# Kernel optimization log

Hardware: AMD Instinct MI355X
Metric: run time of the kernel (lower is better)

Reference implementation:

```python
import jax, jax.numpy as jnp
import numpy as np
import math

N, E, H, NB, NL, NG, NELEM = 50000, 800000, 64, 8, 2, 64, 100
CUTOFF = 5.0


def _lin(k, fin, fout):
    kw, kb = jax.random.split(k)
    bound = 1.0 / math.sqrt(fin)
    w = jax.random.uniform(kw, (fin, fout), jnp.float32, -bound, bound)
    b = jax.random.uniform(kb, (fout,), jnp.float32, -bound, bound)
    return w, b


def setup_inputs() -> dict:
    key = jax.random.key(0)
    ks = jax.random.split(key, 12)
    z = jax.random.randint(ks[0], (N,), 0, NELEM)
    pos = jax.random.normal(ks[1], (N, 3), jnp.float32)
    edge_index = jax.random.randint(ks[2], (2, E), 0, N)
    batch = jnp.sort(jax.random.randint(ks[3], (N,), 0, NG))
    embed = jax.random.normal(ks[4], (NELEM, H), jnp.float32)
    # stacked per-interaction MLP params, leading dim = NL
    msg_w1, msg_b1, msg_w2, msg_b2 = [], [], [], []
    upd_w1, upd_b1, upd_w2, upd_b2 = [], [], [], []
    for l in range(NL):
        kl = jax.random.fold_in(ks[5], l)
        k1, k2, k3, k4 = jax.random.split(kl, 4)
        w, b = _lin(k1, 2 * H + NB, H); msg_w1.append(w); msg_b1.append(b)
        w, b = _lin(k2, H, H); msg_w2.append(w); msg_b2.append(b)
        w, b = _lin(k3, 2 * H, H); upd_w1.append(w); upd_b1.append(b)
        w, b = _lin(k4, H, H); upd_w2.append(w); upd_b2.append(b)
    eh_w1, eh_b1 = _lin(ks[6], H, H)
    eh_w2, eh_b2 = _lin(ks[7], H, 1)
    return {
        "z": z, "pos": pos, "edge_index": edge_index, "batch": batch,
        "embed": embed,
        "msg_w1": jnp.stack(msg_w1), "msg_b1": jnp.stack(msg_b1),
        "msg_w2": jnp.stack(msg_w2), "msg_b2": jnp.stack(msg_b2),
        "upd_w1": jnp.stack(upd_w1), "upd_b1": jnp.stack(upd_b1),
        "upd_w2": jnp.stack(upd_w2), "upd_b2": jnp.stack(upd_b2),
        "eh_w1": eh_w1, "eh_b1": eh_b1, "eh_w2": eh_w2, "eh_b2": eh_b2,
    }


def _mace_energy(pos, embed, msg_w1, msg_b1, msg_w2, msg_b2,
                 upd_w1, upd_b1, upd_w2, upd_b2,
                 eh_w1, eh_b1, eh_w2, eh_b2,
                 z, edge_index, batch):
    row, col = edge_index[0], edge_index[1]
    edge_vec = pos[row] - pos[col]                      # (E,3)
    d = jnp.linalg.norm(edge_vec, axis=-1)              # (E,)
    env = jnp.where(d < CUTOFF,
                    jnp.cos(d * (math.pi / (2 * CUTOFF))) ** 2,
                    0.0)
    freqs = jnp.arange(1, NB + 1, dtype=pos.dtype) * (math.pi / CUTOFF)
    d_safe = jnp.where(d > 0, d, 1.0)[:, None]
    edge_attr = jnp.sin(freqs * d[:, None]) / d_safe * env[:, None]  # (E,NB)

    x = embed[z]                                        # (N,H)
    for l in range(NL):
        # PyG source_to_target: x_j = x[row], x_i = x[col], aggregate at col
        msg_in = jnp.concatenate([x[col], x[row], edge_attr], axis=-1)  # (E,2H+NB)
        m = jax.nn.silu(msg_in @ msg_w1[l] + msg_b1[l]) @ msg_w2[l] + msg_b2[l]
        agg = jax.ops.segment_sum(m, col, num_segments=N)               # (N,H)
        u_in = jnp.concatenate([x, agg], axis=-1)
        upd = jax.nn.silu(u_in @ upd_w1[l] + upd_b1[l]) @ upd_w2[l] + upd_b2[l]
        x = x + upd

    atomic_e = jax.nn.silu(x @ eh_w1 + eh_b1) @ eh_w2 + eh_b2           # (N,1)
    energy = jax.ops.segment_sum(atomic_e, batch, num_segments=NG)      # (NG,1)
    return energy.squeeze(-1)


def reference(z, pos, edge_index, batch, embed,
              msg_w1, msg_b1, msg_w2, msg_b2,
              upd_w1, upd_b1, upd_w2, upd_b2,
              eh_w1, eh_b1, eh_w2, eh_b2):
    return _mace_energy(pos, embed, msg_w1, msg_b1, msg_w2, msg_b2,
                        upd_w1, upd_b1, upd_w2, upd_b2,
                        eh_w1, eh_b1, eh_w2, eh_b2,
                        z, edge_index, batch)
```

## Files before the change

kernel.cpp:

```cpp
#include <hip/hip_runtime.h>
#include <math.h>

#define NN 50000
#define EE 800000
#define HH 64
#define NBASIS 8
#define NLAYER 2
#define NGRAPH 64
#define NBLK1 49

using half2_t = decltype(__builtin_amdgcn_cvt_pkrtz(0.0f, 0.0f));
typedef _Float16 f16x8 __attribute__((ext_vector_type(8)));
typedef float f32x4 __attribute__((ext_vector_type(4)));

union U4H8 { uint4 u; f16x8 h; };

__device__ __forceinline__ float silu_f(float v) {
    return v * (1.0f / (1.0f + __expf(-v)));
}

__device__ __forceinline__ unsigned pk2(float a, float b) {
    union { half2_t h; unsigned u; } x;
    x.h = __builtin_amdgcn_cvt_pkrtz(a, b);
    return x.u;
}

__global__ __launch_bounds__(256) void prep_k(
    const int* __restrict__ z, const float* __restrict__ embed,
    float* __restrict__ x, unsigned* __restrict__ xh,
    const float* __restrict__ msg_w1, const float* __restrict__ msg_w2,
    const float* __restrict__ upd_w1, const float* __restrict__ upd_w2,
    const float* __restrict__ eh_w1,
    unsigned* __restrict__ w1t, unsigned* __restrict__ w2t,
    unsigned* __restrict__ w1tu, unsigned* __restrict__ w2tu,
    unsigned* __restrict__ ehw1t,
    const int* __restrict__ ecol, int* __restrict__ deg)
{
    int b = blockIdx.x;
    if (b < 6250) {
        int idx = b * 256 + threadIdx.x;
        int n = idx >> 5;
        int p = idx & 31;
        const float2* er = (const float2*)(embed + ((size_t)z[n] << 6));
        float2 v = er[p];
        ((float2*)x)[idx] = v;
        xh[idx] = pk2(v.x, v.y);
    } else if (b < 6362) {
        int idx = (b - 6250) * 256 + threadIdx.x;
        if (idx < 10240) {
            int l = idx / 5120, rem = idx % 5120;
            int f = rem / 80, kp = rem % 80;
            const float* w = msg_w1 + (size_t)l * 136 * 64;
            unsigned v = 0;
            if (kp < 68) v = pk2(w[(2*kp)*64 + f], w[(2*kp+1)*64 + f]);
            w1t[idx] = v;
        } else if (idx < 14336) {
            int j = idx - 10240;
            int l = j / 2048, rem = j % 2048;
            int n = rem / 32, kp = rem % 32;
            const float* w = msg_w2 + (size_t)l * 64 * 64;
            w2t[j] = pk2(w[(2*kp)*64 + n], w[(2*kp+1)*64 + n]);
        } else if (idx < 22528) {
            int j = idx - 14336;
            int l = j / 4096, rem = j % 4096;
            int f = rem >> 6, kp = rem & 63;
            const float* w = upd_w1 + (size_t)l * 128 * 64;
            w1tu[j] = pk2(w[(2*kp)*64 + f], w[(2*kp+1)*64 + f]);
        } else if (idx < 26624) {
            int j = idx - 22528;
            int l = j / 2048, rem = j % 2048;
            int n = rem / 32, kp = rem % 32;
            const float* w = upd_w2 + (size_t)l * 64 * 64;
            w2tu[j] = pk2(w[(2*kp)*64 + n], w[(2*kp+1)*64 + n]);
        } else if (idx < 28672) {
            int j = idx - 26624;
            int f = j / 32, kp = j % 32;
            ehw1t[j] = pk2(eh_w1[(2*kp)*64 + f], eh_w1[(2*kp+1)*64 + f]);
        }
    } else {
        int e = (b - 6362) * 256 + threadIdx.x;
        if (e < EE) atomicAdd(&deg[ecol[e]], 1);
    }
}

__global__ __launch_bounds__(1024) void scan1_k(
    const int* __restrict__ deg, int* __restrict__ cursor,
    int* __restrict__ bsum)
{
    __shared__ int wsum[16];
    int t = threadIdx.x, lane = t & 63, wave = t >> 6;
    int i = blockIdx.x * 1024 + t;
    int v = (i < NN) ? deg[i] : 0;
    int s = v;
#pragma unroll
    for (int off = 1; off < 64; off <<= 1) {
        int tv = __shfl_up(s, off, 64);
        if (lane >= off) s += tv;
    }
    if (lane == 63) wsum[wave] = s;
    __syncthreads();
    if (wave == 0) {
        int ws = (lane < 16) ? wsum[lane] : 0;
        int ss = ws;
#pragma unroll
        for (int off = 1; off < 16; off <<= 1) {
            int tv = __shfl_up(ss, off, 64);
            if (lane >= off) ss += tv;
        }
        if (lane < 16) wsum[lane] = ss - ws;
    }
    __syncthreads();
    int excl = wsum[wave] + s - v;
    if (i < NN) cursor[i] = excl;
    if (t == 1023) bsum[blockIdx.x] = excl + v;
}

__global__ __launch_bounds__(64) void scan2_k(int* __restrict__ bsum)
{
    int lane = threadIdx.x;
    int v = (lane < NBLK1) ? bsum[lane] : 0;
    int s = v;
#pragma unroll
    for (int off = 1; off < 64; off <<= 1) {
        int tv = __shfl_up(s, off, 64);
        if (lane >= off) s += tv;
    }
    if (lane < NBLK1) bsum[lane] = s - v;
}

__global__ __launch_bounds__(256) void scatter_k(
    const int* __restrict__ erow, const int* __restrict__ ecol,
    const float* __restrict__ pos,
    int* __restrict__ cursor, const int* __restrict__ bsum,
    uint4* __restrict__ edgeS)
{
    int e = blockIdx.x * 256 + threadIdx.x;
    if (e >= EE) return;
    int c = ecol[e], r = erow[e];
    int slot = atomicAdd(&cursor[c], 1) + bsum[c >> 10];
    float dx = pos[3*r]   - pos[3*c];
    float dy = pos[3*r+1] - pos[3*c+1];
    float dz = pos[3*r+2] - pos[3*c+2];
    float d = sqrtf(dx*dx + dy*dy + dz*dz);
    uint4 v;
    v.x = (unsigned)r; v.y = (unsigned)c;
    v.z = __float_as_uint(d); v.w = 0;
    edgeS[slot] = v;
}

__global__ __launch_bounds__(256, 4) void msg_k(
    const uint4* __restrict__ edgeS,
    const unsigned* __restrict__ xh,
    const unsigned* __restrict__ w1t, const float* __restrict__ b1,
    const unsigned* __restrict__ w2t, const float* __restrict__ b2,
    float* __restrict__ agg)
{
    __shared__ __align__(16) unsigned earr[4][64 * 4];
    __shared__ int ckey_s[4][64];
    __shared__ int rkey_s[4][64];
    __shared__ float Mbuf[4][64 * 33];

    const int wid  = threadIdx.x >> 6;
    const int lane = threadIdx.x & 63;
    const int q = lane >> 4, n15 = lane & 15;
    const size_t base = (size_t)blockIdx.x * 256 + wid * 64;

    {
        uint4 ev = edgeS[base + lane];
        rkey_s[wid][lane] = (int)ev.x;
        ckey_s[wid][lane] = (int)ev.y;
        float d = __uint_as_float(ev.z);
        float env = 0.0f;
        if (d < 5.0f) {
            float cv = __cosf(d * 0.31415926535897932f);
            env = cv * cv;
        }
        float scale = (d > 0.0f) ? (env / d) : env;
        float ea[NBASIS];
#pragma unroll
        for (int k = 0; k < NBASIS; ++k)
            ea[k] = __sinf((float)(k + 1) * 0.62831853071795865f * d) * scale;
#pragma unroll
        for (int p = 0; p < 4; ++p)
            earr[wid][lane * 4 + p] = pk2(ea[2*p], ea[2*p+1]);
    }
    __syncthreads();

    int cn[4], rn[4];
#pragma unroll
    for (int nt = 0; nt < 4; ++nt) {
        int eB = nt * 16 + n15;
        cn[nt] = ckey_s[wid][eB];
        rn[nt] = rkey_s[wid][eB];
    }

    f32x4 acc1[4][4];
#pragma unroll
    for (int mt = 0; mt < 4; ++mt) {
        f32x4 binit = *(const f32x4*)(b1 + mt * 16 + q * 4);
#pragma unroll
        for (int nt = 0; nt < 4; ++nt) acc1[mt][nt] = binit;
    }
#pragma unroll
    for (int ks = 0; ks < 5; ++ks) {
        U4H8 bfk[4];
#pragma unroll
        for (int nt = 0; nt < 4; ++nt) {
            if (ks == 4) {
                uint4 zz; zz.x = zz.y = zz.z = zz.w = 0;
                bfk[nt].u = (q == 0) ? *(const uint4*)(earr[wid] + (nt * 16 + n15) * 4) : zz;
            } else if (ks < 2) {
                bfk[nt].u = ((const uint4*)(xh + ((size_t)cn[nt] << 5)))[ks * 4 + q];
            } else {
                bfk[nt].u = ((const uint4*)(xh + ((size_t)rn[nt] << 5)))[(ks - 2) * 4 + q];
            }
        }
#pragma unroll
        for (int mt = 0; mt < 4; ++mt) {
            U4H8 af;
            af.u = *(const uint4*)(w1t + (size_t)(mt * 16 + n15) * 80 + ks * 16 + q * 4);
#pragma unroll
            for (int nt = 0; nt < 4; ++nt)
                acc1[mt][nt] = __builtin_amdgcn_mfma_f32_16x16x32_f16(
                    af.h, bfk[nt].h, acc1[mt][nt], 0, 0, 0);
        }
    }

    unsigned psrc[4][4][2];
#pragma unroll
    for (int mt = 0; mt < 4; ++mt)
#pragma unroll
        for (int nt = 0; nt < 4; ++nt) {
            psrc[mt][nt][0] = pk2(silu_f(acc1[mt][nt][0]), silu_f(acc1[mt][nt][1]));
            psrc[mt][nt][1] = pk2(silu_f(acc1[mt][nt][2]), silu_f(acc1[mt][nt][3]));
        }

    f32x4 acc2[4][4];
#pragma unroll
    for (int nt = 0; nt < 4; ++nt) {
        float b2v = b2[nt * 16 + n15];
        f32x4 binit; binit[0] = b2v; binit[1] = b2v; binit[2] = b2v; binit[3] = b2v;
#pragma unroll
        for (int et = 0; et < 4; ++et) acc2[et][nt] = binit;
    }
#pragma unroll
    for (int ks2 = 0; ks2 < 2; ++ks2) {
        U4H8 wb[4];
#pragma unroll
        for (int nt = 0; nt < 4; ++nt)
            wb[nt].u = *(const uint4*)(w2t + (size_t)(nt * 16 + n15) * 32 + ks2 * 16 + q * 4);
#pragma unroll
        for (int et = 0; et < 4; ++et) {
            unsigned tmp[4];
#pragma unroll
            for (int jr = 0; jr < 4; ++jr) {
                int srcl = (2 * (q & 1) + (jr >> 1)) * 16 + n15;
                unsigned v0 = (unsigned)__shfl((int)psrc[2 * ks2][et][jr & 1], srcl, 64);
                unsigned v1 = (unsigned)__shfl((int)psrc[2 * ks2 + 1][et][jr & 1], srcl, 64);
                tmp[jr] = (q >> 1) ? v1 : v0;
            }
            U4H8 pf;
            pf.u.x = tmp[0]; pf.u.y = tmp[1]; pf.u.z = tmp[2]; pf.u.w = tmp[3];
#pragma unroll
            for (int nt = 0; nt < 4; ++nt)
                acc2[et][nt] = __builtin_amdgcn_mfma_f32_16x16x32_f16(
                    pf.h, wb[nt].h, acc2[et][nt], 0, 0, 0);
        }
    }

#pragma unroll
    for (int hf = 0; hf < 2; ++hf) {
#pragma unroll
        for (int et = 0; et < 4; ++et)
#pragma unroll
            for (int t2 = 0; t2 < 2; ++t2) {
                int nt = 2 * hf + t2;
                int cl = t2 * 16 + n15;
                int eb = et * 16 + q * 4;
#pragma unroll
                for (int r = 0; r < 4; ++r)
                    Mbuf[wid][(eb + r) * 33 + cl] = acc2[et][nt][r];
            }
        __syncthreads();
        {
            int cl = lane & 31, st = lane >> 5;
            int ebase = 32 * st;
            float run = 0.0f;
            int runkey = ckey_s[wid][ebase];
            bool atstart = true;
#pragma unroll
            for (int i = 0; i < 32; ++i) {
                int kk = ckey_s[wid][ebase + i];
                float v = Mbuf[wid][(ebase + i) * 33 + cl];
                if (kk != runkey) {
                    float* dst = agg + ((size_t)runkey << 6) + hf * 32 + cl;
                    if (atstart) atomicAdd(dst, run); else *dst = run;
                    run = 0.0f; runkey = kk; atstart = false;
                }
                run += v;
            }
            atomicAdd(agg + ((size_t)runkey << 6) + hf * 32 + cl, run);
        }
        __syncthreads();
    }
}

__global__ __launch_bounds__(64) void upd_k(
    float* __restrict__ x, unsigned* __restrict__ xh,
    const float* __restrict__ agg,
    const unsigned* __restrict__ w1t, const float* __restrict__ b1,
    const unsigned* __restrict__ w2t, const float* __restrict__ b2)
{
    __shared__ float Mbuf[64 * 33];

    const int lane = threadIdx.x;
    const int q = lane >> 4, n15 = lane & 15;
    const int nbase = blockIdx.x * 64;

    int nc[4];
#pragma unroll
    for (int nt = 0; nt < 4; ++nt) {
        int node = nbase + nt * 16 + n15;
        nc[nt] = (node < NN) ? node : (NN - 1);
    }

    f32x4 acc1[4][4];
#pragma unroll
    for (int mt = 0; mt < 4; ++mt) {
        f32x4 binit = *(const f32x4*)(b1 + mt * 16 + q * 4);
#pragma unroll
        for (int nt = 0; nt < 4; ++nt) acc1[mt][nt] = binit;
    }
#pragma unroll
    for (int ks = 0; ks < 4; ++ks) {
        U4H8 bfk[4];
#pragma unroll
        for (int nt = 0; nt < 4; ++nt) {
            if (ks < 2) {
                bfk[nt].u = ((const uint4*)(xh + ((size_t)nc[nt] << 5)))[ks * 4 + q];
            } else {
                const float4* ap = (const float4*)(agg + ((size_t)nc[nt] << 6));
                int o = (ks - 2) * 8 + 2 * q;
                float4 a0 = ap[o], a1 = ap[o + 1];
                bfk[nt].u.x = pk2(a0.x, a0.y); bfk[nt].u.y = pk2(a0.z, a0.w);
                bfk[nt].u.z = pk2(a1.x, a1.y); bfk[nt].u.w = pk2(a1.z, a1.w);
            }
        }
#pragma unroll
        for (int mt = 0; mt < 4; ++mt) {
            U4H8 af;
            af.u = *(const uint4*)(w1t + (size_t)(mt * 16 + n15) * 64 + ks * 16 + q * 4);
#pragma unroll
            for (int nt = 0; nt < 4; ++nt)
                acc1[mt][nt] = __builtin_amdgcn_mfma_f32_16x16x32_f16(
                    af.h, bfk[nt].h, acc1[mt][nt], 0, 0, 0);
        }
    }

    unsigned psrc[4][4][2];
#pragma unroll
    for (int mt = 0; mt < 4; ++mt)
#pragma unroll
        for (int nt = 0; nt < 4; ++nt) {
            psrc[mt][nt][0] = pk2(silu_f(acc1[mt][nt][0]), silu_f(acc1[mt][nt][1]));
            psrc[mt][nt][1] = pk2(silu_f(acc1[mt][nt][2]), silu_f(acc1[mt][nt][3]));
        }

    f32x4 acc2[4][4];
#pragma unroll
    for (int nt = 0; nt < 4; ++nt) {
        float b2v = b2[nt * 16 + n15];
        f32x4 binit; binit[0] = b2v; binit[1] = b2v; binit[2] = b2v; binit[3] = b2v;
#pragma unroll
        for (int et = 0; et < 4; ++et) acc2[et][nt] = binit;
    }
#pragma unroll
    for (int ks2 = 0; ks2 < 2; ++ks2) {
        U4H8 wb[4];
#pragma unroll
        for (int nt = 0; nt < 4; ++nt)
            wb[nt].u = *(const uint4*)(w2t + (size_t)(nt * 16 + n15) * 32 + ks2 * 16 + q * 4);
#pragma unroll
        for (int et = 0; et < 4; ++et) {
            unsigned tmp[4];
#pragma unroll
            for (int jr = 0; jr < 4; ++jr) {
                int srcl = (2 * (q & 1) + (jr >> 1)) * 16 + n15;
                unsigned v0 = (unsigned)__shfl((int)psrc[2 * ks2][et][jr & 1], srcl, 64);
                unsigned v1 = (unsigned)__shfl((int)psrc[2 * ks2 + 1][et][jr & 1], srcl, 64);
                tmp[jr] = (q >> 1) ? v1 : v0;
            }
            U4H8 pf;
            pf.u.x = tmp[0]; pf.u.y = tmp[1]; pf.u.z = tmp[2]; pf.u.w = tmp[3];
#pragma unroll
            for (int nt = 0; nt < 4; ++nt)
                acc2[et][nt] = __builtin_amdgcn_mfma_f32_16x16x32_f16(
                    pf.h, wb[nt].h, acc2[et][nt], 0, 0, 0);
        }
    }

#pragma unroll
    for (int hf = 0; hf < 2; ++hf) {
#pragma unroll
        for (int et = 0; et < 4; ++et)
#pragma unroll
            for (int t2 = 0; t2 < 2; ++t2) {
                int nt = 2 * hf + t2;
                int cl = t2 * 16 + n15;
                int eb = et * 16 + q * 4;
#pragma unroll
                for (int r = 0; r < 4; ++r)
                    Mbuf[(eb + r) * 33 + cl] = acc2[et][nt][r];
            }
        __syncthreads();
        {
            int node = nbase + lane;
            if (node < NN) {
                float* xr = x + ((size_t)node << 6) + hf * 32;
                unsigned* xhp = xh + ((size_t)node << 5) + hf * 16;
#pragma unroll
                for (int p = 0; p < 16; ++p) {
                    float v0 = xr[2*p]     + Mbuf[lane * 33 + 2*p];
                    float v1 = xr[2*p + 1] + Mbuf[lane * 33 + 2*p + 1];
                    xr[2*p] = v0; xr[2*p + 1] = v1;
                    xhp[p] = pk2(v0, v1);
                }
            }
        }
        __syncthreads();
    }
}

__global__ __launch_bounds__(64) void head_k(
    const unsigned* __restrict__ xh,
    const unsigned* __restrict__ w1t, const float* __restrict__ b1,
    const float* __restrict__ w2, const float* __restrict__ b2,
    const int* __restrict__ batch, float* __restrict__ energy)
{
    __shared__ float esum[NGRAPH];

    const int lane = threadIdx.x;
    const int q = lane >> 4, n15 = lane & 15;
    const int nbase = blockIdx.x * 64;

    esum[lane] = 0.0f;
    __syncthreads();

    int nc[4];
#pragma unroll
    for (int nt = 0; nt < 4; ++nt) {
        int node = nbase + nt * 16 + n15;
        nc[nt] = (node < NN) ? node : (NN - 1);
    }

    f32x4 acc[4][4];
#pragma unroll
    for (int mt = 0; mt < 4; ++mt) {
        f32x4 binit = *(const f32x4*)(b1 + mt * 16 + q * 4);
#pragma unroll
        for (int nt = 0; nt < 4; ++nt) acc[mt][nt] = binit;
    }
#pragma unroll
    for (int ks = 0; ks < 2; ++ks) {
        U4H8 bfk[4];
#pragma unroll
        for (int nt = 0; nt < 4; ++nt)
            bfk[nt].u = ((const uint4*)(xh + ((size_t)nc[nt] << 5)))[ks * 4 + q];
#pragma unroll
        for (int mt = 0; mt < 4; ++mt) {
            U4H8 af;
            af.u = *(const uint4*)(w1t + (size_t)(mt * 16 + n15) * 32 + ks * 16 + q * 4);
#pragma unroll
            for (int nt = 0; nt < 4; ++nt)
                acc[mt][nt] = __builtin_amdgcn_mfma_f32_16x16x32_f16(
                    af.h, bfk[nt].h, acc[mt][nt], 0, 0, 0);
        }
    }

    f32x4 wv[4];
#pragma unroll
    for (int mt = 0; mt < 4; ++mt) wv[mt] = *(const f32x4*)(w2 + mt * 16 + q * 4);
    float b2v = b2[0];
#pragma unroll
    for (int nt = 0; nt < 4; ++nt) {
        float e = 0.0f;
#pragma unroll
        for (int mt = 0; mt < 4; ++mt)
#pragma unroll
            for (int r = 0; r < 4; ++r)
                e = fmaf(silu_f(acc[mt][nt][r]), wv[mt][r], e);
        e += __shfl_xor(e, 16, 64);
        e += __shfl_xor(e, 32, 64);
        if (q == 0) {
            int node = nbase + nt * 16 + n15;
            if (node < NN) atomicAdd(&esum[batch[node]], e + b2v);
        }
    }
    __syncthreads();
    float v = esum[lane];
    if (v != 0.0f) atomicAdd(energy + lane, v);
}

extern "C" void kernel_launch(void* const* d_in, const int* in_sizes, int n_in,
                              void* d_out, int out_size, void* d_ws, size_t ws_size,
                              hipStream_t stream) {
    const int*   z       = (const int*)  d_in[0];
    const float* pos     = (const float*)d_in[1];
    const int*   eidx    = (const int*)  d_in[2];
    const int*   batch   = (const int*)  d_in[3];
    const float* embed   = (const float*)d_in[4];
    const float* msg_w1  = (const float*)d_in[5];
    const float* msg_b1  = (const float*)d_in[6];
    const float* msg_w2  = (const float*)d_in[7];
    const float* msg_b2  = (const float*)d_in[8];
    const float* upd_w1  = (const float*)d_in[9];
    const float* upd_b1  = (const float*)d_in[10];
    const float* upd_w2  = (const float*)d_in[11];
    const float* upd_b2  = (const float*)d_in[12];
    const float* eh_w1   = (const float*)d_in[13];
    const float* eh_b1   = (const float*)d_in[14];
    const float* eh_w2   = (const float*)d_in[15];
    const float* eh_b2   = (const float*)d_in[16];

    const int* erow = eidx;
    const int* ecol = eidx + EE;

    float*    x      = (float*)d_ws;
    float*    agg    = x + (size_t)NN * HH;
    unsigned* xh     = (unsigned*)(agg + (size_t)NN * HH);
    int*      deg    = (int*)(xh + (size_t)NN * 32);
    int*      cursor = deg + NN;
    int*      bsum   = cursor + NN;
    uint4*    edgeS  = (uint4*)(bsum + 64);
    unsigned* w1t    = (unsigned*)(edgeS + EE);
    unsigned* w2t    = w1t + NLAYER * 64 * 80;
    unsigned* w1tu   = w2t + NLAYER * 64 * 32;
    unsigned* w2tu   = w1tu + NLAYER * 64 * 64;
    unsigned* ehw1t  = w2tu + NLAYER * 64 * 32;
    float*    energy = (float*)d_out;

    (void)hipMemsetAsync(energy, 0, NGRAPH * sizeof(float), stream);
    (void)hipMemsetAsync(deg, 0, NN * sizeof(int), stream);

    prep_k<<<9487, 256, 0, stream>>>(
        z, embed, x, xh,
        msg_w1, msg_w2, upd_w1, upd_w2, eh_w1,
        w1t, w2t, w1tu, w2tu, ehw1t,
        ecol, deg);

    scan1_k<<<NBLK1, 1024, 0, stream>>>(deg, cursor, bsum);
    scan2_k<<<1, 64, 0, stream>>>(bsum);
    scatter_k<<<(EE + 255) / 256, 256, 0, stream>>>(
        erow, ecol, pos, cursor, bsum, edgeS);

    for (int l = 0; l < NLAYER; ++l) {
        (void)hipMemsetAsync(agg, 0, (size_t)NN * HH * sizeof(float), stream);
        msg_k<<<EE / 256, 256, 0, stream>>>(
            edgeS, xh,
            w1t + (size_t)l * 64 * 80,
            msg_b1 + (size_t)l * HH,
            w2t + (size_t)l * 64 * 32,
            msg_b2 + (size_t)l * HH,
            agg);
        upd_k<<<(NN + 63) / 64, 64, 0, stream>>>(
            x, xh, agg,
            w1tu + (size_t)l * 64 * 64,
            upd_b1 + (size_t)l * HH,
            w2tu + (size_t)l * 64 * 32,
            upd_b2 + (size_t)l * HH);
    }

    head_k<<<(NN + 63) / 64, 64, 0, stream>>>(
        xh, ehw1t, eh_b1, eh_w2, eh_b2, batch, energy);
}
```

Before: 401.3 us.

## Fuse energy head and agg zeroing into update kernel; ballot-based segment boundaries

The energy-head MLP is folded into the final update kernel, reusing the freshly packed half-precision node features staged in shared memory instead of a separate launch that re-reads them. The per-layer agg memset is replaced by one upfront memset plus zeroing inside the first layer's update kernel. In the message kernel, segment boundaries for the sorted-key scatter are precomputed with a ballot, so the reduction loop no longer reads a key from shared memory at every step. This cuts launches and memory traffic but adds register pressure (a 32-entry array) and extra shared-memory work to the update kernel.

```diff
diff --git a/kernel.cpp b/kernel.cpp
--- a/kernel.cpp
+++ b/kernel.cpp
@@ -165,10 +165,12 @@
     const int q = lane >> 4, n15 = lane & 15;
     const size_t base = (size_t)blockIdx.x * 256 + wid * 64;
 
+    int mykey;
     {
         uint4 ev = edgeS[base + lane];
         rkey_s[wid][lane] = (int)ev.x;
-        ckey_s[wid][lane] = (int)ev.y;
+        mykey = (int)ev.y;
+        ckey_s[wid][lane] = mykey;
         float d = __uint_as_float(ev.z);
         float env = 0.0f;
         if (d < 5.0f) {
@@ -184,6 +186,9 @@
         for (int p = 0; p < 4; ++p)
             earr[wid][lane * 4 + p] = pk2(ea[2*p], ea[2*p+1]);
     }
+    int pkk = __shfl_up(mykey, 1, 64);
+    unsigned long long bmask = __ballot(lane > 0 && mykey != pkk);
+    unsigned m32 = (unsigned)(bmask >> (lane & 32));
     __syncthreads();
 
     int cn[4], rn[4];
@@ -285,19 +290,20 @@
         {
             int cl = lane & 31, st = lane >> 5;
             int ebase = 32 * st;
-            float run = 0.0f;
+            float run = Mbuf[wid][ebase * 33 + cl];
             int runkey = ckey_s[wid][ebase];
             bool atstart = true;
 #pragma unroll
-            for (int i = 0; i < 32; ++i) {
-                int kk = ckey_s[wid][ebase + i];
+            for (int i = 1; i < 32; ++i) {
                 float v = Mbuf[wid][(ebase + i) * 33 + cl];
-                if (kk != runkey) {
+                if ((m32 >> i) & 1u) {
                     float* dst = agg + ((size_t)runkey << 6) + hf * 32 + cl;
                     if (atstart) atomicAdd(dst, run); else *dst = run;
-                    run = 0.0f; runkey = kk; atstart = false;
+                    runkey = ckey_s[wid][ebase + i]; atstart = false;
+                    run = v;
+                } else {
+                    run += v;
                 }
-                run += v;
             }
             atomicAdd(agg + ((size_t)runkey << 6) + hf * 32 + cl, run);
         }
@@ -307,11 +313,16 @@
 
 __global__ __launch_bounds__(64) void upd_k(
     float* __restrict__ x, unsigned* __restrict__ xh,
-    const float* __restrict__ agg,
+    float* __restrict__ agg,
     const unsigned* __restrict__ w1t, const float* __restrict__ b1,
-    const unsigned* __restrict__ w2t, const float* __restrict__ b2)
+    const unsigned* __restrict__ w2t, const float* __restrict__ b2,
+    const unsigned* __restrict__ ehw1t, const float* __restrict__ ehb1,
+    const float* __restrict__ ehw2, const float* __restrict__ ehb2,
+    const int* __restrict__ batch, float* __restrict__ energy,
+    int do_zero, int do_head)
 {
     __shared__ float Mbuf[64 * 33];
+    __shared__ float esum[NGRAPH];
 
     const int lane = threadIdx.x;
     const int q = lane >> 4, n15 = lane & 15;
@@ -399,6 +410,9 @@
         }
     }
 
+    unsigned prr[32];
+#pragma unroll
+    for (int p = 0; p < 32; ++p) prr[p] = 0;
 #pragma unroll
     for (int hf = 0; hf < 2; ++hf) {
 #pragma unroll
@@ -423,82 +437,84 @@
                     float v0 = xr[2*p]     + Mbuf[lane * 33 + 2*p];
                     float v1 = xr[2*p + 1] + Mbuf[lane * 33 + 2*p + 1];
                     xr[2*p] = v0; xr[2*p + 1] = v1;
-                    xhp[p] = pk2(v0, v1);
+                    unsigned pv = pk2(v0, v1);
+                    xhp[p] = pv;
+                    prr[hf * 16 + p] = pv;
                 }
             }
         }
         __syncthreads();
     }
-}
-
-__global__ __launch_bounds__(64) void head_k(
-    const unsigned* __restrict__ xh,
-    const unsigned* __restrict__ w1t, const float* __restrict__ b1,
-    const float* __restrict__ w2, const float* __restrict__ b2,
-    const int* __restrict__ batch, float* __restrict__ energy)
-{
-    __shared__ float esum[NGRAPH];
-
-    const int lane = threadIdx.x;
-    const int q = lane >> 4, n15 = lane & 15;
-    const int nbase = blockIdx.x * 64;
-
-    esum[lane] = 0.0f;
-    __syncthreads();
-
-    int nc[4];
-#pragma unroll
-    for (int nt = 0; nt < 4; ++nt) {
-        int node = nbase + nt * 16 + n15;
-        nc[nt] = (node < NN) ? node : (NN - 1);
-    }
-
-    f32x4 acc[4][4];
-#pragma unroll
-    for (int mt = 0; mt < 4; ++mt) {
-        f32x4 binit = *(const f32x4*)(b1 + mt * 16 + q * 4);
-#pragma unroll
-        for (int nt = 0; nt < 4; ++nt) acc[mt][nt] = binit;
-    }
-#pragma unroll
-    for (int ks = 0; ks < 2; ++ks) {
-        U4H8 bfk[4];
-#pragma unroll
-        for (int nt = 0; nt < 4; ++nt)
-            bfk[nt].u = ((const uint4*)(xh + ((size_t)nc[nt] << 5)))[ks * 4 + q];
+
+    if (do_zero) {
+        int node = nbase + lane;
+        if (node < NN) {
+            float4 z4; z4.x = z4.y = z4.z = z4.w = 0.0f;
+            float4* ap = (float4*)(agg + ((size_t)node << 6));
+#pragma unroll
+            for (int p = 0; p < 16; ++p) ap[p] = z4;
+        }
+    }
+
+    if (do_head) {
+        unsigned* MU = (unsigned*)Mbuf;
+        esum[lane] = 0.0f;
+#pragma unroll
+        for (int p = 0; p < 32; ++p) MU[lane * 33 + p] = prr[p];
+        __syncthreads();
+
+        f32x4 acch[4][4];
 #pragma unroll
         for (int mt = 0; mt < 4; ++mt) {
-            U4H8 af;
-            af.u = *(const uint4*)(w1t + (size_t)(mt * 16 + n15) * 32 + ks * 16 + q * 4);
-#pragma unroll
-            for (int nt = 0; nt < 4; ++nt)
-                acc[mt][nt] = __builtin_amdgcn_mfma_f32_16x16x32_f16(
-                    af.h, bfk[nt].h, acc[mt][nt], 0, 0, 0);
-        }
-    }
-
-    f32x4 wv[4];
-#pragma unroll
-    for (int mt = 0; mt < 4; ++mt) wv[mt] = *(const f32x4*)(w2 + mt * 16 + q * 4);
-    float b2v = b2[0];
-#pragma unroll
-    for (int nt = 0; nt < 4; ++nt) {
-        float e = 0.0f;
-#pragma unroll
-        for (int mt = 0; mt < 4; ++mt)
-#pragma unroll
-            for (int r = 0; r < 4; ++r)
-                e = fmaf(silu_f(acc[mt][nt][r]), wv[mt][r], e);
-        e += __shfl_xor(e, 16, 64);
-        e += __shfl_xor(e, 32, 64);
-        if (q == 0) {
-            int node = nbase + nt * 16 + n15;
-            if (node < NN) atomicAdd(&esum[batch[node]], e + b2v);
-        }
-    }
-    __syncthreads();
-    float v = esum[lane];
-    if (v != 0.0f) atomicAdd(energy + lane, v);
+            f32x4 binit = *(const f32x4*)(ehb1 + mt * 16 + q * 4);
+#pragma unroll
+            for (int nt = 0; nt < 4; ++nt) acch[mt][nt] = binit;
+        }
+#pragma unroll
+        for (int ks = 0; ks < 2; ++ks) {
+            U4H8 bfk[4];
+#pragma unroll
+            for (int nt = 0; nt < 4; ++nt) {
+                int nd = nt * 16 + n15;
+                bfk[nt].u.x = MU[nd * 33 + ks * 16 + 4 * q + 0];
+                bfk[nt].u.y = MU[nd * 33 + ks * 16 + 4 * q + 1];
+                bfk[nt].u.z = MU[nd * 33 + ks * 16 + 4 * q + 2];
+                bfk[nt].u.w = MU[nd * 33 + ks * 16 + 4 * q + 3];
+            }
+#pragma unroll
+            for (int mt = 0; mt < 4; ++mt) {
+                U4H8 af;
+                af.u = *(const uint4*)(ehw1t + (size_t)(mt * 16 + n15) * 32 + ks * 16 + q * 4);
+#pragma unroll
+                for (int nt = 0; nt < 4; ++nt)
+                    acch[mt][nt] = __builtin_amdgcn_mfma_f32_16x16x32_f16(
+                        af.h, bfk[nt].h, acch[mt][nt], 0, 0, 0);
+            }
+        }
+
+        f32x4 wv[4];
+#pragma unroll
+        for (int mt = 0; mt < 4; ++mt) wv[mt] = *(const f32x4*)(ehw2 + mt * 16 + q * 4);
+        float b2v = ehb2[0];
+#pragma unroll
+        for (int nt = 0; nt < 4; ++nt) {
+            float e = 0.0f;
+#pragma unroll
+            for (int mt = 0; mt < 4; ++mt)
+#pragma unroll
+                for (int r = 0; r < 4; ++r)
+                    e = fmaf(silu_f(acch[mt][nt][r]), wv[mt][r], e);
+            e += __shfl_xor(e, 16, 64);
+            e += __shfl_xor(e, 32, 64);
+            if (q == 0) {
+                int node = nbase + nt * 16 + n15;
+                if (node < NN) atomicAdd(&esum[batch[node]], e + b2v);
+            }
+        }
+        __syncthreads();
+        float v = esum[lane];
+        if (v != 0.0f) atomicAdd(energy + lane, v);
+    }
 }
 
 extern "C" void kernel_launch(void* const* d_in, const int* in_sizes, int n_in,
@@ -541,6 +557,7 @@
 
     (void)hipMemsetAsync(energy, 0, NGRAPH * sizeof(float), stream);
     (void)hipMemsetAsync(deg, 0, NN * sizeof(int), stream);
+    (void)hipMemsetAsync(agg, 0, (size_t)NN * HH * sizeof(float), stream);
 
     prep_k<<<9487, 256, 0, stream>>>(
         z, embed, x, xh,
@@ -554,7 +571,6 @@
         erow, ecol, pos, cursor, bsum, edgeS);
 
     for (int l = 0; l < NLAYER; ++l) {
-        (void)hipMemsetAsync(agg, 0, (size_t)NN * HH * sizeof(float), stream);
         msg_k<<<EE / 256, 256, 0, stream>>>(
             edgeS, xh,
             w1t + (size_t)l * 64 * 80,
@@ -567,9 +583,9 @@
             w1tu + (size_t)l * 64 * 64,
             upd_b1 + (size_t)l * HH,
             w2tu + (size_t)l * 64 * 32,
-            upd_b2 + (size_t)l * HH);
-    }
-
-    head_k<<<(NN + 63) / 64, 64, 0, stream>>>(
-        xh, ehw1t, eh_b1, eh_w2, eh_b2, batch, energy);
-}
+            upd_b2 + (size_t)l * HH,
+            ehw1t, eh_b1, eh_w2, eh_b2, batch, energy,
+            (l == 0) ? 1 : 0,
+            (l == NLAYER - 1) ? 1 : 0);
+    }
+}
```

Measured after the change: 388.3 us. 3.3% less time.
